# Optimization experiments

Hardware: AMD Instinct MI355X
Metric: run time of the kernel (lower is better)

Reference implementation:

```python
import jax, jax.numpy as jnp
import numpy as np

E = 8
DIMS = [512, 1024, 1024, 512]
BATCH = 2048


def _init_w(key, shape):
    a = np.sqrt(6.0 / (shape[-2] * shape[-1]))
    return jax.random.uniform(key, shape, dtype=jnp.float32, minval=-a, maxval=a)


def setup_inputs() -> dict:
    key = jax.random.key(0)
    ks = jax.random.split(key, 8)
    inp = {
        "weight_blend": jax.random.uniform(ks[0], (BATCH, E), dtype=jnp.float32),
        "x": jax.random.normal(ks[1], (BATCH, DIMS[0]), dtype=jnp.float32),
    }
    for i in range(3):
        inp[f"W{i}"] = _init_w(ks[2 + i], (E, DIMS[i + 1], DIMS[i]))
        inp[f"B{i}"] = jnp.zeros((E, DIMS[i + 1], 1), dtype=jnp.float32)
    return inp


def reference(weight_blend, x, W0, B0, W1, B1, W2, B2):
    Ws = [W0, W1, W2]
    Bs = [B0, B1, B2]
    acts = [jax.nn.elu, jax.nn.elu, None]
    for W, B, act in zip(Ws, Bs, acts):
        # dropout p=0 -> identity
        # blended-expert GEMM: sum_e wb[b,e] * (W[e] @ x[b]) == einsum
        t = jnp.einsum("be,eoi,bi->bo", weight_blend, W, x)
        bias = jnp.einsum("be,eo->bo", weight_blend, B[..., 0])
        x = t + bias
        if act is not None:
            x = act(x)
    return x
```

## Files before the change

kernel.cpp:

```cpp
#include <hip/hip_runtime.h>
#include <math.h>

typedef __attribute__((ext_vector_type(8))) short bf16x8;
typedef __attribute__((ext_vector_type(4))) float f32x4;

#define NEXP 8
#define BATCH 2048

__device__ __forceinline__ unsigned short f2bf(float f) {
    union { float f; unsigned u; } v; v.f = f;
    unsigned r = v.u + 0x7FFFu + ((v.u >> 16) & 1u);
    return (unsigned short)(r >> 16);
}

__global__ __launch_bounds__(256) void pack_all(
    const float* __restrict__ W0, const float* __restrict__ W1,
    const float* __restrict__ W2, const float* __restrict__ x,
    unsigned short* __restrict__ W0p, unsigned short* __restrict__ W1p,
    unsigned short* __restrict__ W2p, unsigned short* __restrict__ x0p)
{
    __shared__ float T[128 * 36];
    const int bid = blockIdx.x, t = threadIdx.x;

    if (bid < 10240) {
        const float* W; unsigned short* out; int KB, Din, Dout, U, lin;
        if (bid < 2048)      { W = W0; out = W0p; KB = 16; Din = 512;  Dout = 1024; U = 4; lin = bid; }
        else if (bid < 6144) { W = W1; out = W1p; KB = 32; Din = 1024; Dout = 1024; U = 4; lin = bid - 2048; }
        else                 { W = W2; out = W2p; KB = 32; Din = 1024; Dout = 512;  U = 2; lin = bid - 6144; }
        const int e  = lin & 7;
        const int r  = lin >> 3;
        const int kb = r % KB;
        const int nb = r / KB;
        const int N0 = nb * 16 * U;
        const int K0 = kb * 32;
        for (int it = 0; it < U / 2; ++it) {
            const int idx = t + 256 * it;
            const int nl = idx >> 3, k4 = (idx & 7) * 4;
            float4 v = *(const float4*)(W + ((size_t)e * Dout + N0 + nl) * Din + K0 + k4);
            *(float4*)(T + nl * 36 + k4) = v;
        }
        __syncthreads();
        if (t < 64 * U) {
            const int u = t >> 6, l = t & 63;
            const float* p = T + (u * 16 + (l & 15)) * 36 + (l >> 4) * 8;
            bf16x8 h;
            #pragma unroll
            for (int j = 0; j < 8; ++j) h[j] = (short)f2bf(p[j]);
            *(bf16x8*)(out + (size_t)lin * (U * 512) + t * 8) = h;
        }
    } else {
        const int lin = bid - 10240;
        const int kb = lin & 15, mb = lin >> 4;
        for (int it = 0; it < 4; ++it) {
            const int idx = t + 256 * it;
            const int ml = idx >> 3, k4 = (idx & 7) * 4;
            float4 v = *(const float4*)(x + (size_t)(mb * 128 + ml) * 512 + kb * 32 + k4);
            *(float4*)(T + ml * 36 + k4) = v;
        }
        __syncthreads();
        #pragma unroll
        for (int it = 0; it < 2; ++it) {
            const int s = t + 256 * it;
            const int g = s >> 6, l = s & 63;
            const float* p = T + (g * 16 + (l & 15)) * 36 + (l >> 4) * 8;
            bf16x8 h;
            #pragma unroll
            for (int j = 0; j < 8; ++j) h[j] = (short)f2bf(p[j]);
            *(bf16x8*)(x0p + (size_t)lin * 4096 + s * 8) = h;
        }
    }
}

template<int UP>
__global__ __launch_bounds__(256, 3) void moe_mfma6(
    const unsigned short* __restrict__ Xp,
    const unsigned short* __restrict__ Wp,
    const float* __restrict__ Bias,
    const float* __restrict__ WBl,
    void* __restrict__ Yout,
    int KB, int Dout, int KBn, int act, int packed_out)
{
    constexpr int PSTR = 36;
    __shared__ __align__(16) float lds_f[2 * 64 * PSTR];

    const int tid  = threadIdx.x;
    const int ew   = tid >> 6;
    const int l    = tid & 63;
    const int lh   = l >> 4;
    const int ll   = l & 15;
    const int e0   = 2 * ew;
    const int bx   = blockIdx.x;
    const int by   = blockIdx.y;
    const int m0   = by * 64;
    const int n0   = bx * 32;
    const int mb   = by >> 1;
    const int half = by & 1;

    f32x4 acc0[4][2], acc1[4][2];
    #pragma unroll
    for (int t = 0; t < 4; ++t)
        #pragma unroll
        for (int u = 0; u < 2; ++u)
            #pragma unroll
            for (int i = 0; i < 4; ++i) { acc0[t][u][i] = 0.f; acc1[t][u][i] = 0.f; }

    unsigned aoff[4];
    #pragma unroll
    for (int t = 0; t < 4; ++t)
        aoff[t] = (unsigned)(mb * KB) * 8192u + (unsigned)(half * 4 + t) * 1024u + l * 16u;
    const int nb   = (bx * 2) / UP;
    const int uoff = (bx * 2) % UP;
    unsigned boff0[2], boff1[2];
    #pragma unroll
    for (int u = 0; u < 2; ++u) {
        boff0[u] = (((unsigned)(nb * KB) * 8 + e0) * UP + uoff + u) * 1024u + l * 16u;
        boff1[u] = boff0[u] + UP * 1024u;
    }
    const unsigned astr = 8192u;
    const unsigned bstr = UP * 8192u;
    const char* xc = (const char*)Xp;
    const char* wc = (const char*)Wp;

    bf16x8 aR[2][4], b0R[2][2], b1R[2][2];

    auto LOAD = [&](int s, int kk) {
        const unsigned ab = (unsigned)kk * astr;
        const unsigned bb = (unsigned)kk * bstr;
        #pragma unroll
        for (int t = 0; t < 4; ++t)
            aR[s][t] = *(const bf16x8*)(xc + aoff[t] + ab);
        #pragma unroll
        for (int u = 0; u < 2; ++u) {
            b0R[s][u] = *(const bf16x8*)(wc + boff0[u] + bb);
            b1R[s][u] = *(const bf16x8*)(wc + boff1[u] + bb);
        }
    };
    auto MF = [&](int s) {
        #pragma unroll
        for (int u = 0; u < 2; ++u)
            #pragma unroll
            for (int t = 0; t < 4; ++t) {
                acc0[t][u] = __builtin_amdgcn_mfma_f32_16x16x32_bf16(aR[s][t], b0R[s][u], acc0[t][u], 0, 0, 0);
                acc1[t][u] = __builtin_amdgcn_mfma_f32_16x16x32_bf16(aR[s][t], b1R[s][u], acc1[t][u], 0, 0, 0);
            }
    };

    LOAD(0, 0);
    for (int kk = 0; kk < KB; kk += 2) {
        if (kk + 1 < KB) LOAD(1, kk + 1);
        MF(0);
        if (kk + 2 < KB) LOAD(0, kk + 2);
        MF(1);
    }

    float bi0[2], bi1[2];
    #pragma unroll
    for (int u = 0; u < 2; ++u) {
        const int n = n0 + u * 16 + ll;
        bi0[u] = Bias[(size_t)e0 * Dout + n];
        bi1[u] = Bias[(size_t)(e0 + 1) * Dout + n];
    }

    float* pb = lds_f + (ew & 1) * (64 * PSTR);

    if (ew < 2) {
        #pragma unroll
        for (int t = 0; t < 4; ++t)
            #pragma unroll
            for (int r = 0; r < 4; ++r) {
                const int lm = 16 * t + 4 * lh + r;
                float2 wbp = ((const float2*)(WBl + (size_t)(m0 + lm) * NEXP))[ew];
                #pragma unroll
                for (int u = 0; u < 2; ++u)
                    pb[lm * PSTR + u * 16 + ll] =
                        wbp.x * (acc0[t][u][r] + bi0[u]) + wbp.y * (acc1[t][u][r] + bi1[u]);
            }
    }
    __syncthreads();
    if (ew >= 2) {
        #pragma unroll
        for (int t = 0; t < 4; ++t)
            #pragma unroll
            for (int r = 0; r < 4; ++r) {
                const int lm = 16 * t + 4 * lh + r;
                float2 wbp = ((const float2*)(WBl + (size_t)(m0 + lm) * NEXP))[ew];
                #pragma unroll
                for (int u = 0; u < 2; ++u)
                    pb[lm * PSTR + u * 16 + ll] +=
                        wbp.x * (acc0[t][u][r] + bi0[u]) + wbp.y * (acc1[t][u][r] + bi1[u]);
            }
    }
    __syncthreads();

    float* pb0 = lds_f;
    float* pb1 = lds_f + 64 * PSTR;
    if (packed_out) {
        const int g  = tid >> 6;
        const int c0 = lh * 8;
        const int rowbase = (g * 16 + ll) * PSTR;
        bf16x8 h;
        #pragma unroll
        for (int j = 0; j < 8; ++j) {
            float v = pb0[rowbase + c0 + j] + pb1[rowbase + c0 + j];
            if (act) v = v > 0.f ? v : expm1f(v);
            h[j] = (short)f2bf(v);
        }
        unsigned short* dst = (unsigned short*)Yout +
            ((size_t)(mb * KBn + bx) * 8 + half * 4 + g) * 512 + l * 8;
        *(bf16x8*)dst = h;
    } else {
        #pragma unroll
        for (int it = 0; it < 2; ++it) {
            const int idx = tid + 256 * it;
            const int row = idx >> 3;
            const int c4  = (idx & 7) * 4;
            float4 s = *(const float4*)(pb0 + row * PSTR + c4);
            float4 q = *(const float4*)(pb1 + row * PSTR + c4);
            s.x += q.x; s.y += q.y; s.z += q.z; s.w += q.w;
            if (act) {
                s.x = s.x > 0.f ? s.x : expm1f(s.x);
                s.y = s.y > 0.f ? s.y : expm1f(s.y);
                s.z = s.z > 0.f ? s.z : expm1f(s.z);
                s.w = s.w > 0.f ? s.w : expm1f(s.w);
            }
            *(float4*)((float*)Yout + (size_t)(m0 + row) * Dout + n0 + c4) = s;
        }
    }
}

#define BM 64
#define BNF 64
#define BKF 16
#define PAD 4

__global__ __launch_bounds__(256) void moe_layer_f32(
    const float* __restrict__ X, const float* __restrict__ W,
    const float* __restrict__ Bias, const float* __restrict__ WB,
    float* __restrict__ Y, int Din, int Dout, int act)
{
    __shared__ float As[BKF][BM + PAD];
    __shared__ float Bs[BKF][BNF + PAD];
    const int tid = threadIdx.x;
    const int tm = tid >> 4, tn = tid & 15;
    const int m0 = blockIdx.y * BM, n0 = blockIdx.x * BNF;
    const int lr = tid >> 2, lc = (tid & 3) << 2;
    float acc[4][4] = {};
    const float* xrow  = X  + (size_t)(m0 + lr) * Din;
    const float* wbrow = WB + (size_t)(m0 + lr) * NEXP;
    const float* wrow0 = W  + (size_t)(n0 + lr) * Din;
    for (int e = 0; e < NEXP; ++e) {
        const float wbe = wbrow[e];
        const float* wrow = wrow0 + (size_t)e * Dout * Din;
        for (int k0 = 0; k0 < Din; k0 += BKF) {
            float4 av = *(const float4*)(xrow + k0 + lc);
            float4 bv = *(const float4*)(wrow + k0 + lc);
            __syncthreads();
            As[lc+0][lr] = av.x*wbe; As[lc+1][lr] = av.y*wbe;
            As[lc+2][lr] = av.z*wbe; As[lc+3][lr] = av.w*wbe;
            Bs[lc+0][lr] = bv.x; Bs[lc+1][lr] = bv.y;
            Bs[lc+2][lr] = bv.z; Bs[lc+3][lr] = bv.w;
            __syncthreads();
            #pragma unroll
            for (int k = 0; k < BKF; ++k) {
                float4 a = *(const float4*)&As[k][tm << 2];
                float4 b = *(const float4*)&Bs[k][tn << 2];
                acc[0][0]+=a.x*b.x; acc[0][1]+=a.x*b.y; acc[0][2]+=a.x*b.z; acc[0][3]+=a.x*b.w;
                acc[1][0]+=a.y*b.x; acc[1][1]+=a.y*b.y; acc[1][2]+=a.y*b.z; acc[1][3]+=a.y*b.w;
                acc[2][0]+=a.z*b.x; acc[2][1]+=a.z*b.y; acc[2][2]+=a.z*b.z; acc[2][3]+=a.z*b.w;
                acc[3][0]+=a.w*b.x; acc[3][1]+=a.w*b.y; acc[3][2]+=a.w*b.z; acc[3][3]+=a.w*b.w;
            }
        }
    }
    #pragma unroll
    for (int im = 0; im < 4; ++im) {
        const int m = m0 + (tm << 2) + im;
        const float* wbm = WB + (size_t)m * NEXP;
        float wv[NEXP];
        #pragma unroll
        for (int e = 0; e < NEXP; ++e) wv[e] = wbm[e];
        #pragma unroll
        for (int in = 0; in < 4; ++in) {
            const int n = n0 + (tn << 2) + in;
            float bsum = 0.f;
            #pragma unroll
            for (int e = 0; e < NEXP; ++e) bsum += wv[e] * Bias[(size_t)e * Dout + n];
            float v = acc[im][in] + bsum;
            if (act) v = v > 0.f ? v : expm1f(v);
            acc[im][in] = v;
        }
        float4 o = make_float4(acc[im][0], acc[im][1], acc[im][2], acc[im][3]);
        *(float4*)(Y + (size_t)m * Dout + n0 + (tn << 2)) = o;
    }
}

extern "C" void kernel_launch(void* const* d_in, const int* in_sizes, int n_in,
                              void* d_out, int out_size, void* d_ws, size_t ws_size,
                              hipStream_t stream)
{
    (void)in_sizes; (void)n_in; (void)out_size;
    const float* wb = (const float*)d_in[0];
    const float* x  = (const float*)d_in[1];
    const float* W0 = (const float*)d_in[2];
    const float* B0 = (const float*)d_in[3];
    const float* W1 = (const float*)d_in[4];
    const float* B1 = (const float*)d_in[5];
    const float* W2 = (const float*)d_in[6];
    const float* B2 = (const float*)d_in[7];
    float* out = (float*)d_out;

    const size_t NW0 = (size_t)8*1024*512, NW1 = (size_t)8*1024*1024, NW2 = (size_t)8*512*1024;
    const size_t NX0 = (size_t)BATCH*512, NX1 = (size_t)BATCH*1024;
    const size_t need = (NW0 + NW1 + NW2 + NX0 + 2 * NX1) * 2;

    if (ws_size >= need) {
        unsigned short* W0p = (unsigned short*)d_ws;
        unsigned short* W1p = W0p + NW0;
        unsigned short* W2p = W1p + NW1;
        unsigned short* x0p = W2p + NW2;
        unsigned short* x1p = x0p + NX0;
        unsigned short* x2p = x1p + NX1;
        pack_all<<<10496, 256, 0, stream>>>(W0, W1, W2, x, W0p, W1p, W2p, x0p);
        moe_mfma6<4><<<dim3(32, 32), 256, 0, stream>>>(x0p, W0p, B0, wb, x1p, 16, 1024, 32, 1, 1);
        moe_mfma6<4><<<dim3(32, 32), 256, 0, stream>>>(x1p, W1p, B1, wb, x2p, 32, 1024, 32, 1, 1);
        moe_mfma6<2><<<dim3(16, 32), 256, 0, stream>>>(x2p, W2p, B2, wb, out, 32, 512,  0, 0, 0);
    } else {
        float* x1 = (float*)d_ws;
        float* x2 = x1 + (size_t)BATCH * 1024;
        moe_layer_f32<<<dim3(1024/BNF, BATCH/BM), 256, 0, stream>>>(x,  W0, B0, wb, x1, 512,  1024, 1);
        moe_layer_f32<<<dim3(1024/BNF, BATCH/BM), 256, 0, stream>>>(x1, W1, B1, wb, x2, 1024, 1024, 1);
        moe_layer_f32<<<dim3(512/BNF,  BATCH/BM), 256, 0, stream>>>(x2, W2, B2, wb, out, 1024, 512,  0);
    }
}
```

Baseline: 203.4 us.

## Use 512-thread blocks sharing weights across two M halves with deeper prefetch

```diff
diff --git a/kernel.cpp b/kernel.cpp
--- a/kernel.cpp
+++ b/kernel.cpp
@@ -72,7 +72,7 @@
 }
 
 template<int UP>
-__global__ __launch_bounds__(256, 3) void moe_mfma6(
+__global__ __launch_bounds__(512, 2) void moe_mfma7(
     const unsigned short* __restrict__ Xp,
     const unsigned short* __restrict__ Wp,
     const float* __restrict__ Bias,
@@ -81,20 +81,21 @@
     int KB, int Dout, int KBn, int act, int packed_out)
 {
     constexpr int PSTR = 36;
-    __shared__ __align__(16) float lds_f[2 * 64 * PSTR];
-
-    const int tid  = threadIdx.x;
-    const int ew   = tid >> 6;
-    const int l    = tid & 63;
-    const int lh   = l >> 4;
-    const int ll   = l & 15;
-    const int e0   = 2 * ew;
-    const int bx   = blockIdx.x;
-    const int by   = blockIdx.y;
-    const int m0   = by * 64;
-    const int n0   = bx * 32;
-    const int mb   = by >> 1;
-    const int half = by & 1;
+    __shared__ __align__(16) float lds_f[4 * 64 * PSTR];
+
+    const int tid = threadIdx.x;
+    const int wv  = tid >> 6;
+    const int mh  = wv >> 2;
+    const int ep  = wv & 3;
+    const int l   = tid & 63;
+    const int lh  = l >> 4;
+    const int ll  = l & 15;
+    const int e0  = 2 * ep;
+    const int bx  = blockIdx.x;
+    const int by  = blockIdx.y;
+    const int m0  = by * 128;
+    const int n0  = bx * 32;
+    const int mb  = by;
 
     f32x4 acc0[4][2], acc1[4][2];
     #pragma unroll
@@ -107,7 +108,7 @@
     unsigned aoff[4];
     #pragma unroll
     for (int t = 0; t < 4; ++t)
-        aoff[t] = (unsigned)(mb * KB) * 8192u + (unsigned)(half * 4 + t) * 1024u + l * 16u;
+        aoff[t] = (unsigned)(mb * KB) * 8192u + (unsigned)(mh * 4 + t) * 1024u + l * 16u;
     const int nb   = (bx * 2) / UP;
     const int uoff = (bx * 2) % UP;
     unsigned boff0[2], boff1[2];
@@ -121,7 +122,7 @@
     const char* xc = (const char*)Xp;
     const char* wc = (const char*)Wp;
 
-    bf16x8 aR[2][4], b0R[2][2], b1R[2][2];
+    bf16x8 aR[4][4], b0R[4][2], b1R[4][2];
 
     auto LOAD = [&](int s, int kk) {
         const unsigned ab = (unsigned)kk * astr;
@@ -136,6 +137,7 @@
         }
     };
     auto MF = [&](int s) {
+        __builtin_amdgcn_s_setprio(1);
         #pragma unroll
         for (int u = 0; u < 2; ++u)
             #pragma unroll
@@ -143,15 +145,19 @@
                 acc0[t][u] = __builtin_amdgcn_mfma_f32_16x16x32_bf16(aR[s][t], b0R[s][u], acc0[t][u], 0, 0, 0);
                 acc1[t][u] = __builtin_amdgcn_mfma_f32_16x16x32_bf16(aR[s][t], b1R[s][u], acc1[t][u], 0, 0, 0);
             }
+        __builtin_amdgcn_s_setprio(0);
     };
 
-    LOAD(0, 0);
-    for (int kk = 0; kk < KB; kk += 2) {
-        if (kk + 1 < KB) LOAD(1, kk + 1);
-        MF(0);
-        if (kk + 2 < KB) LOAD(0, kk + 2);
-        MF(1);
-    }
+    LOAD(0, 0); LOAD(1, 1); LOAD(2, 2);
+    int kk = 0;
+    for (; kk + 4 < KB; kk += 4) {
+        LOAD(3, kk + 3); MF(0);
+        LOAD(0, kk + 4); MF(1);
+        LOAD(1, kk + 5); MF(2);
+        LOAD(2, kk + 6); MF(3);
+    }
+    LOAD(3, KB - 1);
+    MF(0); MF(1); MF(2); MF(3);
 
     float bi0[2], bi1[2];
     #pragma unroll
@@ -161,15 +167,15 @@
         bi1[u] = Bias[(size_t)(e0 + 1) * Dout + n];
     }
 
-    float* pb = lds_f + (ew & 1) * (64 * PSTR);
-
-    if (ew < 2) {
+    float* pb = lds_f + (mh * 2 + (ep & 1)) * (64 * PSTR);
+
+    if (ep < 2) {
         #pragma unroll
         for (int t = 0; t < 4; ++t)
             #pragma unroll
             for (int r = 0; r < 4; ++r) {
                 const int lm = 16 * t + 4 * lh + r;
-                float2 wbp = ((const float2*)(WBl + (size_t)(m0 + lm) * NEXP))[ew];
+                float2 wbp = ((const float2*)(WBl + (size_t)(m0 + mh * 64 + lm) * NEXP))[ep];
                 #pragma unroll
                 for (int u = 0; u < 2; ++u)
                     pb[lm * PSTR + u * 16 + ll] =
@@ -177,13 +183,13 @@
             }
     }
     __syncthreads();
-    if (ew >= 2) {
+    if (ep >= 2) {
         #pragma unroll
         for (int t = 0; t < 4; ++t)
             #pragma unroll
             for (int r = 0; r < 4; ++r) {
                 const int lm = 16 * t + 4 * lh + r;
-                float2 wbp = ((const float2*)(WBl + (size_t)(m0 + lm) * NEXP))[ew];
+                float2 wbp = ((const float2*)(WBl + (size_t)(m0 + mh * 64 + lm) * NEXP))[ep];
                 #pragma unroll
                 for (int u = 0; u < 2; ++u)
                     pb[lm * PSTR + u * 16 + ll] +=
@@ -192,30 +198,34 @@
     }
     __syncthreads();
 
-    float* pb0 = lds_f;
-    float* pb1 = lds_f + 64 * PSTR;
     if (packed_out) {
-        const int g  = tid >> 6;
-        const int c0 = lh * 8;
-        const int rowbase = (g * 16 + ll) * PSTR;
+        const int g   = wv;
+        const int mh2 = g >> 2;
+        const int lr  = (g & 3) * 16 + ll;
+        const float* q0 = lds_f + (mh2 * 2 + 0) * (64 * PSTR) + lr * PSTR + lh * 8;
+        const float* q1 = lds_f + (mh2 * 2 + 1) * (64 * PSTR) + lr * PSTR + lh * 8;
         bf16x8 h;
         #pragma unroll
         for (int j = 0; j < 8; ++j) {
-            float v = pb0[rowbase + c0 + j] + pb1[rowbase + c0 + j];
+            float v = q0[j] + q1[j];
             if (act) v = v > 0.f ? v : expm1f(v);
             h[j] = (short)f2bf(v);
         }
         unsigned short* dst = (unsigned short*)Yout +
-            ((size_t)(mb * KBn + bx) * 8 + half * 4 + g) * 512 + l * 8;
+            ((size_t)(mb * KBn + bx) * 8 + g) * 512 + l * 8;
         *(bf16x8*)dst = h;
     } else {
         #pragma unroll
         for (int it = 0; it < 2; ++it) {
-            const int idx = tid + 256 * it;
+            const int idx = tid + 512 * it;
             const int row = idx >> 3;
             const int c4  = (idx & 7) * 4;
-            float4 s = *(const float4*)(pb0 + row * PSTR + c4);
-            float4 q = *(const float4*)(pb1 + row * PSTR + c4);
+            const int mh2 = row >> 6;
+            const int lr  = row & 63;
+            const float* q0 = lds_f + (mh2 * 2 + 0) * (64 * PSTR) + lr * PSTR + c4;
+            const float* q1 = lds_f + (mh2 * 2 + 1) * (64 * PSTR) + lr * PSTR + c4;
+            float4 s = *(const float4*)q0;
+            float4 q = *(const float4*)q1;
             s.x += q.x; s.y += q.y; s.z += q.z; s.w += q.w;
             if (act) {
                 s.x = s.x > 0.f ? s.x : expm1f(s.x);
@@ -320,9 +330,9 @@
         unsigned short* x1p = x0p + NX0;
         unsigned short* x2p = x1p + NX1;
         pack_all<<<10496, 256, 0, stream>>>(W0, W1, W2, x, W0p, W1p, W2p, x0p);
-        moe_mfma6<4><<<dim3(32, 32), 256, 0, stream>>>(x0p, W0p, B0, wb, x1p, 16, 1024, 32, 1, 1);
-        moe_mfma6<4><<<dim3(32, 32), 256, 0, stream>>>(x1p, W1p, B1, wb, x2p, 32, 1024, 32, 1, 1);
-        moe_mfma6<2><<<dim3(16, 32), 256, 0, stream>>>(x2p, W2p, B2, wb, out, 32, 512,  0, 0, 0);
+        moe_mfma7<4><<<dim3(32, 16), 512, 0, stream>>>(x0p, W0p, B0, wb, x1p, 16, 1024, 32, 1, 1);
+        moe_mfma7<4><<<dim3(32, 16), 512, 0, stream>>>(x1p, W1p, B1, wb, x2p, 32, 1024, 32, 1, 1);
+        moe_mfma7<2><<<dim3(16, 16), 512, 0, stream>>>(x2p, W2p, B2, wb, out, 32, 512,  0, 0, 0);
     } else {
         float* x1 = (float*)d_ws;
         float* x2 = x1 + (size_t)BATCH * 1024;
```

New measurement: 204.6 us. Within noise of the previous version (+0.6%).
